# Performance work log

Measured on AMD Instinct MI355X. Metric: run time of the kernel, lower is better.

Reference implementation:

```python
import jax, jax.numpy as jnp
import numpy as np


def setup_inputs() -> dict:
    key = jax.random.key(0)
    ks = jax.random.split(key, 8)
    B, L, E, U = 32, 2048, 1024, 1024
    s = 0.02
    return {
        "dec_hidden": jax.random.normal(ks[0], (B, E), jnp.float32),
        "enc_output": jax.random.normal(ks[1], (B, L, E), jnp.float32),
        "prev_coverage": jax.random.uniform(ks[2], (B, L, 1), jnp.float32),
        "Ws_k": jax.random.normal(ks[3], (E, U), jnp.float32) * s,
        "Ws_b": jnp.zeros((U,), jnp.float32),
        "Wh_k": jax.random.normal(ks[4], (E, U), jnp.float32) * s,
        "Wh_b": jnp.zeros((U,), jnp.float32),
        "Wc_k": jax.random.normal(ks[5], (1, U), jnp.float32) * s,
        "Wc_b": jnp.zeros((U,), jnp.float32),
        "V_k": jax.random.normal(ks[6], (U, 1), jnp.float32) * s,
        "V_b": jnp.zeros((1,), jnp.float32),
        "enc_pad_mask": jnp.ones((B, L), jnp.int32),
        "use_coverage": 1,
    }


def reference(dec_hidden, enc_output, prev_coverage, Ws_k, Ws_b, Wh_k, Wh_b,
              Wc_k, Wc_b, V_k, V_b, enc_pad_mask, use_coverage):
    # projections: [B,L,U] + [B,1,U] (+ [B,L,U] coverage term)
    pre = jnp.einsum('ble,eu->blu', enc_output, Ws_k) + Ws_b \
        + (dec_hidden @ Wh_k + Wh_b)[:, None, :]
    if use_coverage:
        pre = pre + (prev_coverage @ Wc_k + Wc_b)
    score = jnp.tanh(pre) @ V_k + V_b              # [B, L, 1]
    mask = enc_pad_mask.astype(score.dtype)        # [B, L]
    masked_score = (score[..., 0] * mask)[..., None]  # [B, L, 1]
    attention_weights = jax.nn.softmax(masked_score, axis=1)
    coverage = attention_weights + prev_coverage if use_coverage else attention_weights
    context_vector = jnp.sum(attention_weights * enc_output, axis=1)  # [B, E]
    return (context_vector, attention_weights, coverage)
```

## Files before the change

### kernel.cpp

```cpp
#include <hip/hip_runtime.h>
#include <hip/hip_bf16.h>
#include <math.h>

typedef float f32x4 __attribute__((ext_vector_type(4)));
typedef short short8 __attribute__((ext_vector_type(8)));
typedef unsigned short u16x8 __attribute__((ext_vector_type(8)));

static __device__ __forceinline__ unsigned short f2bf(float f) {
    unsigned u = __builtin_bit_cast(unsigned, f);
    unsigned r = (u + 0x7FFFu + ((u >> 16) & 1u)) >> 16;
    return (unsigned short)r;
}
static __device__ __forceinline__ float bf2f(unsigned short h) {
    unsigned u = ((unsigned)h) << 16;
    return __builtin_bit_cast(float, u);
}
static __device__ __forceinline__ float fast_tanh(float x) {
    float ax = fminf(fmaxf(x, -9.f), 9.f);
    float e = __expf(2.f * ax);
    return 1.f - 2.f / (e + 1.f);
}

#define GLD16(g, l) __builtin_amdgcn_global_load_lds(                        \
    (const __attribute__((address_space(1))) void*)(g),                      \
    (__attribute__((address_space(3))) void*)(l), 16, 0, 0)

__global__ __launch_bounds__(256) void conv_kernel(const float* __restrict__ in,
                                                   unsigned short* __restrict__ out) {
    size_t g = ((size_t)blockIdx.x * 256 + threadIdx.x) * 16;
    const f32x4* p = (const f32x4*)(in + g);
    f32x4 v0 = p[0], v1 = p[1], v2 = p[2], v3 = p[3];
    u16x8 w0, w1;
    w0[0] = f2bf(v0.x); w0[1] = f2bf(v0.y); w0[2] = f2bf(v0.z); w0[3] = f2bf(v0.w);
    w0[4] = f2bf(v1.x); w0[5] = f2bf(v1.y); w0[6] = f2bf(v1.z); w0[7] = f2bf(v1.w);
    w1[0] = f2bf(v2.x); w1[1] = f2bf(v2.y); w1[2] = f2bf(v2.z); w1[3] = f2bf(v2.w);
    w1[4] = f2bf(v3.x); w1[5] = f2bf(v3.y); w1[6] = f2bf(v3.z); w1[7] = f2bf(v3.w);
    *(u16x8*)(out + g) = w0;
    *(u16x8*)(out + g + 8) = w1;
}

__global__ __launch_bounds__(256) void wst_kernel(const float* __restrict__ ws,
                                                  unsigned short* __restrict__ wst) {
    __shared__ unsigned short tile[64][65];
    const int e0 = blockIdx.x * 64, u0 = blockIdx.y * 64;
    const int tid = threadIdx.x;
#pragma unroll
    for (int i = 0; i < 16; i++) {
        int idx = i * 256 + tid;
        int r = idx >> 6, c = idx & 63;
        tile[r][c] = f2bf(ws[(size_t)(e0 + r) * 1024 + u0 + c]);
    }
    __syncthreads();
#pragma unroll
    for (int i = 0; i < 16; i++) {
        int idx = i * 256 + tid;
        int r = idx >> 6, c = idx & 63;
        wst[(size_t)(u0 + r) * 1024 + e0 + c] = tile[c][r];
    }
}

__global__ __launch_bounds__(256) void base_kernel(const float* __restrict__ dh,
                                                   const float* __restrict__ whk,
                                                   float* __restrict__ base) {
    __shared__ float dS[128];
    const int b = blockIdx.x, e0 = blockIdx.y * 128, tid = threadIdx.x;
    if (tid < 128) dS[tid] = dh[b * 1024 + e0 + tid];
    __syncthreads();
    f32x4 acc = {0.f, 0.f, 0.f, 0.f};
#pragma unroll 4
    for (int e = 0; e < 128; e++)
        acc += dS[e] * *(const f32x4*)(whk + (size_t)(e0 + e) * 1024 + tid * 4);
    float* o = base + b * 1024 + tid * 4;
    atomicAdd(o + 0, acc.x);
    atomicAdd(o + 1, acc.y);
    atomicAdd(o + 2, acc.z);
    atomicAdd(o + 3, acc.w);
}

#define BM 128
#define BN 128
#define BK 32

__global__ __launch_bounds__(256) void score_gemm_fast(
    const unsigned short* __restrict__ encB,
    const unsigned short* __restrict__ wst,
    const float* __restrict__ base,
    const float* __restrict__ cov,
    const float* __restrict__ wc,
    const float* __restrict__ vk,
    const float* __restrict__ wsb, const float* __restrict__ whb,
    const float* __restrict__ wcb,
    const int* __restrict__ ucov,
    float* __restrict__ score)
{
    __shared__ unsigned short As[BM * BK];
    __shared__ unsigned short Bs[BN * BK];
    __shared__ float covS[BM];

    const int tid  = threadIdx.x;
    const int u0   = blockIdx.x * BN;
    const int row0 = blockIdx.y * BM;
    const int b    = row0 >> 11;
    const int use_cov = *ucov;

    if (tid < BM) covS[tid] = use_cov ? cov[row0 + tid] : 0.f;

    const int lane = tid & 63;
    const int wid  = tid >> 6;
    const int wm   = wid >> 1, wn = wid & 1;
    const int l16  = lane & 15, quad = lane >> 4;

    const int f0 = tid, f1 = 256 + tid;
    const int rA0 = f0 >> 2, rA1 = f1 >> 2;
    const int cA0 = ((f0 & 3) - rA0 - (rA0 >> 2)) & 3;
    const int cA1 = ((f1 & 3) - rA1 - (rA1 >> 2)) & 3;
    const unsigned short* pA0 = encB + (size_t)(row0 + rA0) * 1024 + cA0 * 8;
    const unsigned short* pA1 = encB + (size_t)(row0 + rA1) * 1024 + cA1 * 8;
    const unsigned short* pB0 = wst + (size_t)(u0 + rA0) * 1024 + cA0 * 8;
    const unsigned short* pB1 = wst + (size_t)(u0 + rA1) * 1024 + cA1 * 8;
    unsigned short* dA0 = As + f0 * 8;
    unsigned short* dA1 = As + f1 * 8;
    unsigned short* dB0 = Bs + f0 * 8;
    unsigned short* dB1 = Bs + f1 * 8;

    int offA[4], offB[4];
#pragma unroll
    for (int t = 0; t < 4; t++) {
        int ra = wm * 64 + t * 16 + l16;
        offA[t] = (ra * 4 + ((quad + ra + (ra >> 2)) & 3)) * 8;
        int rb = wn * 64 + t * 16 + l16;
        offB[t] = (rb * 4 + ((quad + rb + (rb >> 2)) & 3)) * 8;
    }

    f32x4 acc[4][4] = {};

    for (int kk = 0; kk < 1024 / BK; kk++) {
        __syncthreads();
        GLD16(pA0, dA0);
        GLD16(pA1, dA1);
        GLD16(pB0, dB0);
        GLD16(pB1, dB1);
        pA0 += BK; pA1 += BK; pB0 += BK; pB1 += BK;
        __syncthreads();

        short8 a[4], bb[4];
#pragma unroll
        for (int t = 0; t < 4; t++) {
            a[t]  = *(const short8*)&As[offA[t]];
            bb[t] = *(const short8*)&Bs[offB[t]];
        }
#pragma unroll
        for (int i = 0; i < 4; i++)
#pragma unroll
            for (int j = 0; j < 4; j++)
                acc[i][j] = __builtin_amdgcn_mfma_f32_16x16x32_bf16(a[i], bb[j], acc[i][j], 0, 0, 0);
    }

    float basev[4], wcv[4], vv[4];
#pragma unroll
    for (int j = 0; j < 4; j++) {
        int u = u0 + wn * 64 + j * 16 + l16;
        basev[j] = base[b * 1024 + u] + wsb[u] + whb[u] + (use_cov ? wcb[u] : 0.f);
        wcv[j]   = use_cov ? wc[u] : 0.f;
        vv[j]    = vk[u];
    }
#pragma unroll
    for (int i = 0; i < 4; i++) {
        float part[4] = {0.f, 0.f, 0.f, 0.f};
#pragma unroll
        for (int r = 0; r < 4; r++) {
            int rl = wm * 64 + i * 16 + quad * 4 + r;
            float cv = covS[rl];
#pragma unroll
            for (int j = 0; j < 4; j++) {
                float pre = acc[i][j][r] + basev[j] + cv * wcv[j];
                part[r] += fast_tanh(pre) * vv[j];
            }
        }
#pragma unroll
        for (int r = 0; r < 4; r++) {
            float v = part[r];
            v += __shfl_xor(v, 1);
            v += __shfl_xor(v, 2);
            v += __shfl_xor(v, 4);
            v += __shfl_xor(v, 8);
            if (l16 == 0)
                atomicAdd(&score[row0 + wm * 64 + i * 16 + quad * 4 + r], v);
        }
    }
}

#define LDT 40
__global__ __launch_bounds__(256) void score_gemm_f32(
    const float* __restrict__ enc, const unsigned short* __restrict__ wst,
    const float* __restrict__ base, const float* __restrict__ cov,
    const float* __restrict__ wc, const float* __restrict__ vk,
    const float* __restrict__ wsb, const float* __restrict__ whb,
    const float* __restrict__ wcb,
    const int* __restrict__ ucov, float* __restrict__ score)
{
    __shared__ unsigned short As[BM * LDT];
    __shared__ unsigned short Bs[BN * LDT];
    __shared__ float covS[BM];
    const int tid = threadIdx.x;
    const int u0 = blockIdx.x * BN, row0 = blockIdx.y * BM;
    const int b = row0 >> 11;
    const int use_cov = *ucov;
    if (tid < BM) covS[tid] = use_cov ? cov[row0 + tid] : 0.f;
    const int lane = tid & 63, wid = tid >> 6;
    const int wm = wid >> 1, wn = wid & 1;
    const int l16 = lane & 15, quad = lane >> 4;
    f32x4 acc[4][4] = {};
    for (int k0 = 0; k0 < 1024; k0 += BK) {
        __syncthreads();
#pragma unroll
        for (int i = 0; i < 4; i++) {
            int f = i * 256 + tid;
            int r = f >> 3, c4 = f & 7;
            const float* p = enc + (size_t)(row0 + r) * 1024 + k0 + c4 * 4;
            ushort4 w;
            w.x = f2bf(p[0]); w.y = f2bf(p[1]); w.z = f2bf(p[2]); w.w = f2bf(p[3]);
            *(ushort4*)&As[r * LDT + c4 * 4] = w;
        }
#pragma unroll
        for (int i = 0; i < 2; i++) {
            int f = i * 256 + tid;
            int r = f >> 2, c8 = f & 3;
            uint4 w = *(const uint4*)(wst + (size_t)(u0 + r) * 1024 + k0 + c8 * 8);
            *(uint4*)&Bs[r * LDT + c8 * 8] = w;
        }
        __syncthreads();
        short8 a[4], bb[4];
#pragma unroll
        for (int t = 0; t < 4; t++) {
            a[t]  = *(const short8*)&As[(wm * 64 + t * 16 + l16) * LDT + quad * 8];
            bb[t] = *(const short8*)&Bs[(wn * 64 + t * 16 + l16) * LDT + quad * 8];
        }
#pragma unroll
        for (int i = 0; i < 4; i++)
#pragma unroll
            for (int j = 0; j < 4; j++)
                acc[i][j] = __builtin_amdgcn_mfma_f32_16x16x32_bf16(a[i], bb[j], acc[i][j], 0, 0, 0);
    }
    float basev[4], wcv[4], vv[4];
#pragma unroll
    for (int j = 0; j < 4; j++) {
        int u = u0 + wn * 64 + j * 16 + l16;
        basev[j] = base[b * 1024 + u] + wsb[u] + whb[u] + (use_cov ? wcb[u] : 0.f);
        wcv[j] = use_cov ? wc[u] : 0.f;
        vv[j] = vk[u];
    }
#pragma unroll
    for (int i = 0; i < 4; i++) {
        float part[4] = {0.f, 0.f, 0.f, 0.f};
#pragma unroll
        for (int r = 0; r < 4; r++) {
            float cv = covS[wm * 64 + i * 16 + quad * 4 + r];
#pragma unroll
            for (int j = 0; j < 4; j++)
                part[r] += fast_tanh(acc[i][j][r] + basev[j] + cv * wcv[j]) * vv[j];
        }
#pragma unroll
        for (int r = 0; r < 4; r++) {
            float v = part[r];
            v += __shfl_xor(v, 1);
            v += __shfl_xor(v, 2);
            v += __shfl_xor(v, 4);
            v += __shfl_xor(v, 8);
            if (l16 == 0)
                atomicAdd(&score[row0 + wm * 64 + i * 16 + quad * 4 + r], v);
        }
    }
}

__global__ __launch_bounds__(1024) void softmax_kernel(
    const float* __restrict__ score, const float* __restrict__ vb,
    const int* __restrict__ mask, const float* __restrict__ cov,
    const int* __restrict__ ucov,
    float* __restrict__ attn_out, float* __restrict__ cov_out)
{
    __shared__ float redA[16], redB[16];
    __shared__ float bc0, bc1;
    const int b = blockIdx.x, tid = threadIdx.x;
    const int i0 = b * 2048 + tid, i1 = i0 + 1024;
    const float vbv = vb[0];
    const int uc = *ucov;

    float s0 = (score[i0] + vbv) * (float)mask[i0];
    float s1 = (score[i1] + vbv) * (float)mask[i1];

    float m = fmaxf(s0, s1);
#pragma unroll
    for (int off = 1; off < 64; off <<= 1) m = fmaxf(m, __shfl_xor(m, off));
    if ((tid & 63) == 0) redA[tid >> 6] = m;
    __syncthreads();
    if (tid < 16) {
        float v = redA[tid];
#pragma unroll
        for (int off = 1; off < 16; off <<= 1) v = fmaxf(v, __shfl_xor(v, off));
        if (tid == 0) bc0 = v;
    }
    __syncthreads();
    const float M = bc0;

    float e0 = __expf(s0 - M), e1 = __expf(s1 - M);
    float s = e0 + e1;
#pragma unroll
    for (int off = 1; off < 64; off <<= 1) s += __shfl_xor(s, off);
    if ((tid & 63) == 0) redB[tid >> 6] = s;
    __syncthreads();
    if (tid < 16) {
        float v = redB[tid];
#pragma unroll
        for (int off = 1; off < 16; off <<= 1) v += __shfl_xor(v, off);
        if (tid == 0) bc1 = v;
    }
    __syncthreads();
    const float inv = 1.f / bc1;

    float a0 = e0 * inv, a1 = e1 * inv;
    attn_out[i0] = a0;
    attn_out[i1] = a1;
    cov_out[i0] = a0 + (uc ? cov[i0] : 0.f);
    cov_out[i1] = a1 + (uc ? cov[i1] : 0.f);
}

__global__ __launch_bounds__(256) void context_bf16(const unsigned short* __restrict__ encB,
                                                    const float* __restrict__ attn,
                                                    float* __restrict__ ctx) {
    __shared__ float aS[128];
    const int b = blockIdx.x, lc = blockIdx.y, tid = threadIdx.x;
    const int l0 = lc * 128;
    if (tid < 128) aS[tid] = attn[b * 2048 + l0 + tid];
    __syncthreads();
    const int e8 = (tid & 127) * 8, r0 = tid >> 7;
    float acc[8] = {};
#pragma unroll 4
    for (int l = r0; l < 128; l += 2) {
        u16x8 w = *(const u16x8*)(encB + (size_t)(b * 2048 + l0 + l) * 1024 + e8);
        float a = aS[l];
#pragma unroll
        for (int j = 0; j < 8; j++) acc[j] = fmaf(a, bf2f(w[j]), acc[j]);
    }
    float* o = ctx + b * 1024 + e8;
#pragma unroll
    for (int j = 0; j < 8; j++) atomicAdd(o + j, acc[j]);
}

__global__ __launch_bounds__(256) void context_f32(const float* __restrict__ enc,
                                                   const float* __restrict__ attn,
                                                   float* __restrict__ ctx) {
    __shared__ float aS[128];
    const int b = blockIdx.x, lc = blockIdx.y, tid = threadIdx.x;
    const int l0 = lc * 128;
    if (tid < 128) aS[tid] = attn[b * 2048 + l0 + tid];
    __syncthreads();
    const float* p = enc + ((size_t)(b * 2048 + l0)) * 1024 + tid * 4;
    f32x4 acc = {0.f, 0.f, 0.f, 0.f};
#pragma unroll 4
    for (int l = 0; l < 128; l++) acc += *(const f32x4*)(p + (size_t)l * 1024) * aS[l];
    float* o = ctx + b * 1024 + tid * 4;
    atomicAdd(o + 0, acc.x);
    atomicAdd(o + 1, acc.y);
    atomicAdd(o + 2, acc.z);
    atomicAdd(o + 3, acc.w);
}

extern "C" void kernel_launch(void* const* d_in, const int* in_sizes, int n_in,
                              void* d_out, int out_size, void* d_ws, size_t ws_size,
                              hipStream_t stream) {
    const float* dec_hidden = (const float*)d_in[0];
    const float* enc        = (const float*)d_in[1];
    const float* prev_cov   = (const float*)d_in[2];
    const float* Ws_k       = (const float*)d_in[3];
    const float* Ws_b       = (const float*)d_in[4];
    const float* Wh_k       = (const float*)d_in[5];
    const float* Wh_b       = (const float*)d_in[6];
    const float* Wc_k       = (const float*)d_in[7];
    const float* Wc_b       = (const float*)d_in[8];
    const float* V_k        = (const float*)d_in[9];
    const float* V_b        = (const float*)d_in[10];
    const int*   mask       = (const int*)d_in[11];
    const int*   ucov       = (const int*)d_in[12];

    float* out_ctx  = (float*)d_out;
    float* out_attn = out_ctx + 32 * 1024;
    float* out_cov  = out_attn + 65536;

    char* ws = (char*)d_ws;
    unsigned short* wst = (unsigned short*)ws;
    float* base  = (float*)(ws + 2097152);
    float* score = (float*)(ws + 2097152 + 131072);
    unsigned short* encB = (unsigned short*)(ws + 2490368);
    const size_t need_fast = 2490368 + (size_t)32 * 2048 * 1024 * 2;

    hipMemsetAsync(score, 0, 65536 * sizeof(float), stream);
    hipMemsetAsync(base, 0, 32 * 1024 * sizeof(float), stream);
    hipMemsetAsync(out_ctx, 0, 32 * 1024 * sizeof(float), stream);

    wst_kernel<<<dim3(16, 16), 256, 0, stream>>>(Ws_k, wst);
    base_kernel<<<dim3(32, 8), 256, 0, stream>>>(dec_hidden, Wh_k, base);

    if (ws_size >= need_fast) {
        conv_kernel<<<16384, 256, 0, stream>>>(enc, encB);
        score_gemm_fast<<<dim3(8, 512), 256, 0, stream>>>(
            encB, wst, base, prev_cov, Wc_k, V_k, Ws_b, Wh_b, Wc_b, ucov, score);
        softmax_kernel<<<32, 1024, 0, stream>>>(score, V_b, mask, prev_cov, ucov, out_attn, out_cov);
        context_bf16<<<dim3(32, 16), 256, 0, stream>>>(encB, out_attn, out_ctx);
    } else {
        score_gemm_f32<<<dim3(8, 512), 256, 0, stream>>>(
            enc, wst, base, prev_cov, Wc_k, V_k, Ws_b, Wh_b, Wc_b, ucov, score);
        softmax_kernel<<<32, 1024, 0, stream>>>(score, V_b, mask, prev_cov, ucov, out_attn, out_cov);
        context_f32<<<dim3(32, 16), 256, 0, stream>>>(enc, out_attn, out_ctx);
    }
}
```

Before: 693.8 us.

## Replace atomics and memsets with partial-sum planes and fuse prep kernels

Merges the fp32-to-bf16 conversion, the weight transpose and the base projection into one prep launch. The base, score and context sums now go into per-block partial planes that are reduced downstream, so atomics and memsets are no longer needed. The GEMM grid is reordered so row blocks vary fastest, and a ctx_reduce kernel is added. In exchange there is extra partial-buffer traffic and one more launch, and L2 reuse of the weight tile may change with the new grid order.

```diff
diff --git a/kernel.cpp b/kernel.cpp
--- a/kernel.cpp
+++ b/kernel.cpp
@@ -25,56 +25,54 @@
     (const __attribute__((address_space(1))) void*)(g),                      \
     (__attribute__((address_space(3))) void*)(l), 16, 0, 0)
 
-__global__ __launch_bounds__(256) void conv_kernel(const float* __restrict__ in,
-                                                   unsigned short* __restrict__ out) {
-    size_t g = ((size_t)blockIdx.x * 256 + threadIdx.x) * 16;
-    const f32x4* p = (const f32x4*)(in + g);
-    f32x4 v0 = p[0], v1 = p[1], v2 = p[2], v3 = p[3];
-    u16x8 w0, w1;
-    w0[0] = f2bf(v0.x); w0[1] = f2bf(v0.y); w0[2] = f2bf(v0.z); w0[3] = f2bf(v0.w);
-    w0[4] = f2bf(v1.x); w0[5] = f2bf(v1.y); w0[6] = f2bf(v1.z); w0[7] = f2bf(v1.w);
-    w1[0] = f2bf(v2.x); w1[1] = f2bf(v2.y); w1[2] = f2bf(v2.z); w1[3] = f2bf(v2.w);
-    w1[4] = f2bf(v3.x); w1[5] = f2bf(v3.y); w1[6] = f2bf(v3.z); w1[7] = f2bf(v3.w);
-    *(u16x8*)(out + g) = w0;
-    *(u16x8*)(out + g + 8) = w1;
-}
-
-__global__ __launch_bounds__(256) void wst_kernel(const float* __restrict__ ws,
-                                                  unsigned short* __restrict__ wst) {
+__global__ __launch_bounds__(256) void prep_kernel(
+    const float* __restrict__ enc, unsigned short* __restrict__ encB,
+    const float* __restrict__ ws, unsigned short* __restrict__ wst,
+    const float* __restrict__ dh, const float* __restrict__ whk,
+    float* __restrict__ base_part)
+{
     __shared__ unsigned short tile[64][65];
-    const int e0 = blockIdx.x * 64, u0 = blockIdx.y * 64;
-    const int tid = threadIdx.x;
-#pragma unroll
-    for (int i = 0; i < 16; i++) {
-        int idx = i * 256 + tid;
-        int r = idx >> 6, c = idx & 63;
-        tile[r][c] = f2bf(ws[(size_t)(e0 + r) * 1024 + u0 + c]);
-    }
-    __syncthreads();
-#pragma unroll
-    for (int i = 0; i < 16; i++) {
-        int idx = i * 256 + tid;
-        int r = idx >> 6, c = idx & 63;
-        wst[(size_t)(u0 + r) * 1024 + e0 + c] = tile[c][r];
-    }
-}
-
-__global__ __launch_bounds__(256) void base_kernel(const float* __restrict__ dh,
-                                                   const float* __restrict__ whk,
-                                                   float* __restrict__ base) {
     __shared__ float dS[128];
-    const int b = blockIdx.x, e0 = blockIdx.y * 128, tid = threadIdx.x;
-    if (tid < 128) dS[tid] = dh[b * 1024 + e0 + tid];
-    __syncthreads();
-    f32x4 acc = {0.f, 0.f, 0.f, 0.f};
+    const int bid = blockIdx.x, tid = threadIdx.x;
+
+    if (bid < 16384) {
+        const size_t base0 = (size_t)bid * 4096;
+#pragma unroll
+        for (int i = 0; i < 4; i++) {
+            size_t g = base0 + (size_t)i * 1024 + tid * 4;
+            f32x4 v = *(const f32x4*)(enc + g);
+            ushort4 w;
+            w.x = f2bf(v.x); w.y = f2bf(v.y); w.z = f2bf(v.z); w.w = f2bf(v.w);
+            *(ushort4*)(encB + g) = w;
+        }
+    } else if (bid < 16640) {
+        const int b2 = bid - 16384;
+        const int e0 = (b2 & 15) * 64, u0 = (b2 >> 4) * 64;
+#pragma unroll
+        for (int i = 0; i < 16; i++) {
+            int idx = i * 256 + tid;
+            int r = idx >> 6, c = idx & 63;
+            tile[r][c] = f2bf(ws[(size_t)(e0 + r) * 1024 + u0 + c]);
+        }
+        __syncthreads();
+#pragma unroll
+        for (int i = 0; i < 16; i++) {
+            int idx = i * 256 + tid;
+            int r = idx >> 6, c = idx & 63;
+            wst[(size_t)(u0 + r) * 1024 + e0 + c] = tile[c][r];
+        }
+    } else {
+        const int b3 = bid - 16640;
+        const int b = b3 & 31, ec = b3 >> 5;
+        const int e0 = ec * 128;
+        if (tid < 128) dS[tid] = dh[b * 1024 + e0 + tid];
+        __syncthreads();
+        f32x4 acc = {0.f, 0.f, 0.f, 0.f};
 #pragma unroll 4
-    for (int e = 0; e < 128; e++)
-        acc += dS[e] * *(const f32x4*)(whk + (size_t)(e0 + e) * 1024 + tid * 4);
-    float* o = base + b * 1024 + tid * 4;
-    atomicAdd(o + 0, acc.x);
-    atomicAdd(o + 1, acc.y);
-    atomicAdd(o + 2, acc.z);
-    atomicAdd(o + 3, acc.w);
+        for (int e = 0; e < 128; e++)
+            acc += dS[e] * *(const f32x4*)(whk + (size_t)(e0 + e) * 1024 + tid * 4);
+        *(f32x4*)(base_part + (size_t)ec * 32768 + b * 1024 + tid * 4) = acc;
+    }
 }
 
 #define BM 128
@@ -84,22 +82,23 @@
 __global__ __launch_bounds__(256) void score_gemm_fast(
     const unsigned short* __restrict__ encB,
     const unsigned short* __restrict__ wst,
-    const float* __restrict__ base,
+    const float* __restrict__ base_part,
     const float* __restrict__ cov,
     const float* __restrict__ wc,
     const float* __restrict__ vk,
     const float* __restrict__ wsb, const float* __restrict__ whb,
     const float* __restrict__ wcb,
     const int* __restrict__ ucov,
-    float* __restrict__ score)
+    float* __restrict__ score_part)
 {
     __shared__ unsigned short As[BM * BK];
     __shared__ unsigned short Bs[BN * BK];
     __shared__ float covS[BM];
+    __shared__ float sred[2][BM];
 
     const int tid  = threadIdx.x;
-    const int u0   = blockIdx.x * BN;
-    const int row0 = blockIdx.y * BM;
+    const int row0 = blockIdx.x * BM;
+    const int u0   = blockIdx.y * BN;
     const int b    = row0 >> 11;
     const int use_cov = *ucov;
 
@@ -160,7 +159,10 @@
 #pragma unroll
     for (int j = 0; j < 4; j++) {
         int u = u0 + wn * 64 + j * 16 + l16;
-        basev[j] = base[b * 1024 + u] + wsb[u] + whb[u] + (use_cov ? wcb[u] : 0.f);
+        float bsum = wsb[u] + whb[u] + (use_cov ? wcb[u] : 0.f);
+#pragma unroll
+        for (int p = 0; p < 8; p++) bsum += base_part[p * 32768 + b * 1024 + u];
+        basev[j] = bsum;
         wcv[j]   = use_cov ? wc[u] : 0.f;
         vv[j]    = vk[u];
     }
@@ -169,13 +171,10 @@
         float part[4] = {0.f, 0.f, 0.f, 0.f};
 #pragma unroll
         for (int r = 0; r < 4; r++) {
-            int rl = wm * 64 + i * 16 + quad * 4 + r;
-            float cv = covS[rl];
-#pragma unroll
-            for (int j = 0; j < 4; j++) {
-                float pre = acc[i][j][r] + basev[j] + cv * wcv[j];
-                part[r] += fast_tanh(pre) * vv[j];
-            }
+            float cv = covS[wm * 64 + i * 16 + quad * 4 + r];
+#pragma unroll
+            for (int j = 0; j < 4; j++)
+                part[r] += fast_tanh(acc[i][j][r] + basev[j] + cv * wcv[j]) * vv[j];
         }
 #pragma unroll
         for (int r = 0; r < 4; r++) {
@@ -184,16 +183,18 @@
             v += __shfl_xor(v, 2);
             v += __shfl_xor(v, 4);
             v += __shfl_xor(v, 8);
-            if (l16 == 0)
-                atomicAdd(&score[row0 + wm * 64 + i * 16 + quad * 4 + r], v);
-        }
-    }
+            if (l16 == 0) sred[wn][wm * 64 + i * 16 + quad * 4 + r] = v;
+        }
+    }
+    __syncthreads();
+    if (tid < BM)
+        score_part[(size_t)blockIdx.y * 65536 + row0 + tid] = sred[0][tid] + sred[1][tid];
 }
 
 #define LDT 40
 __global__ __launch_bounds__(256) void score_gemm_f32(
     const float* __restrict__ enc, const unsigned short* __restrict__ wst,
-    const float* __restrict__ base, const float* __restrict__ cov,
+    const float* __restrict__ base_part, const float* __restrict__ cov,
     const float* __restrict__ wc, const float* __restrict__ vk,
     const float* __restrict__ wsb, const float* __restrict__ whb,
     const float* __restrict__ wcb,
@@ -203,7 +204,7 @@
     __shared__ unsigned short Bs[BN * LDT];
     __shared__ float covS[BM];
     const int tid = threadIdx.x;
-    const int u0 = blockIdx.x * BN, row0 = blockIdx.y * BM;
+    const int row0 = blockIdx.x * BM, u0 = blockIdx.y * BN;
     const int b = row0 >> 11;
     const int use_cov = *ucov;
     if (tid < BM) covS[tid] = use_cov ? cov[row0 + tid] : 0.f;
@@ -246,7 +247,10 @@
 #pragma unroll
     for (int j = 0; j < 4; j++) {
         int u = u0 + wn * 64 + j * 16 + l16;
-        basev[j] = base[b * 1024 + u] + wsb[u] + whb[u] + (use_cov ? wcb[u] : 0.f);
+        float bsum = wsb[u] + whb[u] + (use_cov ? wcb[u] : 0.f);
+#pragma unroll
+        for (int p = 0; p < 8; p++) bsum += base_part[p * 32768 + b * 1024 + u];
+        basev[j] = bsum;
         wcv[j] = use_cov ? wc[u] : 0.f;
         vv[j] = vk[u];
     }
@@ -274,7 +278,8 @@
 }
 
 __global__ __launch_bounds__(1024) void softmax_kernel(
-    const float* __restrict__ score, const float* __restrict__ vb,
+    const float* __restrict__ score_part, int nplanes,
+    const float* __restrict__ vb,
     const int* __restrict__ mask, const float* __restrict__ cov,
     const int* __restrict__ ucov,
     float* __restrict__ attn_out, float* __restrict__ cov_out)
@@ -286,8 +291,13 @@
     const float vbv = vb[0];
     const int uc = *ucov;
 
-    float s0 = (score[i0] + vbv) * (float)mask[i0];
-    float s1 = (score[i1] + vbv) * (float)mask[i1];
+    float s0 = 0.f, s1 = 0.f;
+    for (int p = 0; p < nplanes; p++) {
+        s0 += score_part[(size_t)p * 65536 + i0];
+        s1 += score_part[(size_t)p * 65536 + i1];
+    }
+    s0 = (s0 + vbv) * (float)mask[i0];
+    s1 = (s1 + vbv) * (float)mask[i1];
 
     float m = fmaxf(s0, s1);
 #pragma unroll
@@ -327,8 +337,9 @@
 
 __global__ __launch_bounds__(256) void context_bf16(const unsigned short* __restrict__ encB,
                                                     const float* __restrict__ attn,
-                                                    float* __restrict__ ctx) {
+                                                    float* __restrict__ ctx_part) {
     __shared__ float aS[128];
+    __shared__ float cred[1024];
     const int b = blockIdx.x, lc = blockIdx.y, tid = threadIdx.x;
     const int l0 = lc * 128;
     if (tid < 128) aS[tid] = attn[b * 2048 + l0 + tid];
@@ -336,15 +347,31 @@
     const int e8 = (tid & 127) * 8, r0 = tid >> 7;
     float acc[8] = {};
 #pragma unroll 4
-    for (int l = r0; l < 128; l += 2) {
+    for (int l = r0 * 64; l < r0 * 64 + 64; l++) {
         u16x8 w = *(const u16x8*)(encB + (size_t)(b * 2048 + l0 + l) * 1024 + e8);
         float a = aS[l];
 #pragma unroll
         for (int j = 0; j < 8; j++) acc[j] = fmaf(a, bf2f(w[j]), acc[j]);
     }
-    float* o = ctx + b * 1024 + e8;
-#pragma unroll
-    for (int j = 0; j < 8; j++) atomicAdd(o + j, acc[j]);
+    if (r0 == 1) {
+#pragma unroll
+        for (int j = 0; j < 8; j++) cred[e8 + j] = acc[j];
+    }
+    __syncthreads();
+    if (r0 == 0) {
+        float* o = ctx_part + (size_t)lc * 32768 + b * 1024 + e8;
+#pragma unroll
+        for (int j = 0; j < 8; j++) o[j] = acc[j] + cred[e8 + j];
+    }
+}
+
+__global__ __launch_bounds__(1024) void ctx_reduce(const float* __restrict__ ctx_part,
+                                                   float* __restrict__ out_ctx) {
+    const int b = blockIdx.x, e = threadIdx.x;
+    float s = 0.f;
+#pragma unroll
+    for (int p = 0; p < 16; p++) s += ctx_part[(size_t)p * 32768 + b * 1024 + e];
+    out_ctx[b * 1024 + e] = s;
 }
 
 __global__ __launch_bounds__(256) void context_f32(const float* __restrict__ enc,
@@ -364,6 +391,43 @@
     atomicAdd(o + 1, acc.y);
     atomicAdd(o + 2, acc.z);
     atomicAdd(o + 3, acc.w);
+}
+
+__global__ __launch_bounds__(256) void prep2_kernel(
+    const float* __restrict__ ws, unsigned short* __restrict__ wst,
+    const float* __restrict__ dh, const float* __restrict__ whk,
+    float* __restrict__ base_part)
+{
+    __shared__ unsigned short tile[64][65];
+    __shared__ float dS[128];
+    const int bid = blockIdx.x, tid = threadIdx.x;
+    if (bid < 256) {
+        const int e0 = (bid & 15) * 64, u0 = (bid >> 4) * 64;
+#pragma unroll
+        for (int i = 0; i < 16; i++) {
+            int idx = i * 256 + tid;
+            int r = idx >> 6, c = idx & 63;
+            tile[r][c] = f2bf(ws[(size_t)(e0 + r) * 1024 + u0 + c]);
+        }
+        __syncthreads();
+#pragma unroll
+        for (int i = 0; i < 16; i++) {
+            int idx = i * 256 + tid;
+            int r = idx >> 6, c = idx & 63;
+            wst[(size_t)(u0 + r) * 1024 + e0 + c] = tile[c][r];
+        }
+    } else {
+        const int b3 = bid - 256;
+        const int b = b3 & 31, ec = b3 >> 5;
+        const int e0 = ec * 128;
+        if (tid < 128) dS[tid] = dh[b * 1024 + e0 + tid];
+        __syncthreads();
+        f32x4 acc = {0.f, 0.f, 0.f, 0.f};
+#pragma unroll 4
+        for (int e = 0; e < 128; e++)
+            acc += dS[e] * *(const f32x4*)(whk + (size_t)(e0 + e) * 1024 + tid * 4);
+        *(f32x4*)(base_part + (size_t)ec * 32768 + b * 1024 + tid * 4) = acc;
+    }
 }
 
 extern "C" void kernel_launch(void* const* d_in, const int* in_sizes, int n_in,
@@ -389,28 +453,26 @@
 
     char* ws = (char*)d_ws;
     unsigned short* wst = (unsigned short*)ws;
-    float* base  = (float*)(ws + 2097152);
-    float* score = (float*)(ws + 2097152 + 131072);
-    unsigned short* encB = (unsigned short*)(ws + 2490368);
-    const size_t need_fast = 2490368 + (size_t)32 * 2048 * 1024 * 2;
-
-    hipMemsetAsync(score, 0, 65536 * sizeof(float), stream);
-    hipMemsetAsync(base, 0, 32 * 1024 * sizeof(float), stream);
-    hipMemsetAsync(out_ctx, 0, 32 * 1024 * sizeof(float), stream);
-
-    wst_kernel<<<dim3(16, 16), 256, 0, stream>>>(Ws_k, wst);
-    base_kernel<<<dim3(32, 8), 256, 0, stream>>>(dec_hidden, Wh_k, base);
+    float* base_part  = (float*)(ws + 2097152);
+    float* score_part = (float*)(ws + 3145728);
+    float* ctx_part   = score_part;
+    unsigned short* encB = (unsigned short*)(ws + 5242880);
+    const size_t need_fast = 5242880 + (size_t)32 * 2048 * 1024 * 2;
 
     if (ws_size >= need_fast) {
-        conv_kernel<<<16384, 256, 0, stream>>>(enc, encB);
-        score_gemm_fast<<<dim3(8, 512), 256, 0, stream>>>(
-            encB, wst, base, prev_cov, Wc_k, V_k, Ws_b, Wh_b, Wc_b, ucov, score);
-        softmax_kernel<<<32, 1024, 0, stream>>>(score, V_b, mask, prev_cov, ucov, out_attn, out_cov);
-        context_bf16<<<dim3(32, 16), 256, 0, stream>>>(encB, out_attn, out_ctx);
+        prep_kernel<<<16896, 256, 0, stream>>>(enc, encB, Ws_k, wst, dec_hidden, Wh_k, base_part);
+        score_gemm_fast<<<dim3(512, 8), 256, 0, stream>>>(
+            encB, wst, base_part, prev_cov, Wc_k, V_k, Ws_b, Wh_b, Wc_b, ucov, score_part);
+        softmax_kernel<<<32, 1024, 0, stream>>>(score_part, 8, V_b, mask, prev_cov, ucov, out_attn, out_cov);
+        context_bf16<<<dim3(32, 16), 256, 0, stream>>>(encB, out_attn, ctx_part);
+        ctx_reduce<<<32, 1024, 0, stream>>>(ctx_part, out_ctx);
     } else {
-        score_gemm_f32<<<dim3(8, 512), 256, 0, stream>>>(
-            enc, wst, base, prev_cov, Wc_k, V_k, Ws_b, Wh_b, Wc_b, ucov, score);
-        softmax_kernel<<<32, 1024, 0, stream>>>(score, V_b, mask, prev_cov, ucov, out_attn, out_cov);
+        hipMemsetAsync(score_part, 0, 65536 * sizeof(float), stream);
+        hipMemsetAsync(out_ctx, 0, 32 * 1024 * sizeof(float), stream);
+        prep2_kernel<<<512, 256, 0, stream>>>(Ws_k, wst, dec_hidden, Wh_k, base_part);
+        score_gemm_f32<<<dim3(512, 8), 256, 0, stream>>>(
+            enc, wst, base_part, prev_cov, Wc_k, V_k, Ws_b, Wh_b, Wc_b, ucov, score_part);
+        softmax_kernel<<<32, 1024, 0, stream>>>(score_part, 1, V_b, mask, prev_cov, ucov, out_attn, out_cov);
         context_f32<<<dim3(32, 16), 256, 0, stream>>>(enc, out_attn, out_ctx);
     }
 }
```

Result: faster. 668.8 us (-3.6%).
